# Performance work log

Measured on AMD Instinct MI355X. Metric: run time of the kernel, lower is better.

## Reference

```python
import jax, jax.numpy as jnp
import numpy as np

NUM_NEURONS = 8192
INPUT_SIZE = 512
OUTPUT_SIZE = 512
TAU = 10.0
G = 1.5


def setup_inputs() -> dict:
    key = jax.random.key(0)
    k1, k2, k3, k4, k5 = jax.random.split(key, 5)
    inputs = jax.random.normal(k1, (INPUT_SIZE,), dtype=jnp.float32)
    potentials = jax.random.normal(k2, (1, NUM_NEURONS), dtype=jnp.float32)
    # parameters, matching the torch init scales
    W_in = jax.random.normal(k3, (INPUT_SIZE, NUM_NEURONS), dtype=jnp.float32) * 0.1
    synapses = jax.random.normal(k4, (NUM_NEURONS, NUM_NEURONS), dtype=jnp.float32) / np.sqrt(NUM_NEURONS).astype(np.float32)
    W_out = jax.random.normal(k5, (NUM_NEURONS, OUTPUT_SIZE), dtype=jnp.float32) / np.float32(NUM_NEURONS)
    return {"inputs": inputs, "potentials": potentials, "W_in": W_in,
            "synapses": synapses, "W_out": W_out}


def reference(inputs, potentials, W_in, synapses, W_out):
    # input_map: bias-free linear, then unsqueeze to [1, N]
    drive = (inputs @ W_in)[None, :]                      # [1, N]
    # Neurons: continuous-time leaky integrator (FORCE-style)
    rates = jnp.tanh(potentials)                          # [1, N]
    pot_new = potentials + (-potentials + G * (rates @ synapses) + drive) / TAU
    gen_net = jnp.tanh(pot_new)                           # [1, N]
    # read_out: bias-free linear
    output = gen_net @ W_out                              # [1, output_size]
    return (output, pot_new)
```

## Files before the change

### kernel.cpp

```cpp
#include <hip/hip_runtime.h>
#include <math.h>

#define N_NEU   8192
#define IN_SZ   512
#define OUT_SZ  512
#define N4      (N_NEU / 4)
#define OUT4    (OUT_SZ / 4)
#define KPB     128
#define WPB     8
#define SYN_TILES (N_NEU / KPB)
#define K2_ROWS 64
#define K2_BLKS (N_NEU / K2_ROWS)
constexpr float TAU_INV = 0.1f;
constexpr float G_GAIN  = 1.5f;

__global__ __launch_bounds__(256)
void accum_kernel(const float* __restrict__ pot,
                  const float* __restrict__ inputs,
                  const float* __restrict__ synapses,
                  const float* __restrict__ W_in,
                  float4* __restrict__ P4,
                  float* __restrict__ out) {
    __shared__ float xs[KPB + WPB];
    const int bx = blockIdx.x, by = blockIdx.y;
    const int tid = threadIdx.x;
    const int k0 = by * KPB;
    const int w0 = by * WPB;
    if (tid < KPB)                xs[tid] = G_GAIN * tanhf(pot[k0 + tid]);
    else if (tid < KPB + WPB)     xs[tid] = inputs[w0 + (tid - KPB)];
    if (bx == 0 && by == 0 && tid < 128)
        ((float4*)out)[tid] = make_float4(0.f, 0.f, 0.f, 0.f);
    __syncthreads();

    const int col4 = bx * 256 + tid;
    const float4* Sp = (const float4*)synapses + (size_t)k0 * N4 + col4;
    const float4* Wp = (const float4*)W_in     + (size_t)w0 * N4 + col4;

    float4 acc = make_float4(0.f, 0.f, 0.f, 0.f);
#pragma unroll 8
    for (int i = 0; i < KPB; ++i) {
        float  s = xs[i];
        float4 m = Sp[(size_t)i * N4];
        acc.x = fmaf(s, m.x, acc.x);
        acc.y = fmaf(s, m.y, acc.y);
        acc.z = fmaf(s, m.z, acc.z);
        acc.w = fmaf(s, m.w, acc.w);
    }
#pragma unroll
    for (int i = 0; i < WPB; ++i) {
        float  s = xs[KPB + i];
        float4 m = Wp[(size_t)i * N4];
        acc.x = fmaf(s, m.x, acc.x);
        acc.y = fmaf(s, m.y, acc.y);
        acc.z = fmaf(s, m.z, acc.z);
        acc.w = fmaf(s, m.w, acc.w);
    }
    P4[(size_t)by * N4 + col4] = acc;
}

__global__ __launch_bounds__(256)
void finish_kernel(const float* __restrict__ pot,
                   const float* __restrict__ P,
                   const float* __restrict__ W_out,
                   float* __restrict__ out) {
    __shared__ float  red[256];
    __shared__ float  xs[K2_ROWS];
    __shared__ float4 hi[128];
    const int b = blockIdx.x;
    const int t = threadIdx.x;
    const int k0 = b * K2_ROWS;
    const int r = t & 63;
    const int q = t >> 6;

    float s = 0.f;
#pragma unroll
    for (int p = 0; p < 16; ++p)
        s += P[(size_t)(q * 16 + p) * N_NEU + k0 + r];
    red[t] = s;
    __syncthreads();

    if (t < K2_ROWS) {
        float drive = red[t] + red[64 + t] + red[128 + t] + red[192 + t];
        float pv = pot[k0 + t];
        float pn = pv + (drive - pv) * TAU_INV;
        out[OUT_SZ + k0 + t] = pn;
        xs[t] = tanhf(pn);
    }
    __syncthreads();

    const int c4 = t & 127;
    const int h  = t >> 7;
    const float4* Wp = (const float4*)W_out + (size_t)(k0 + h * 32) * OUT4 + c4;
    float4 acc = make_float4(0.f, 0.f, 0.f, 0.f);
#pragma unroll 8
    for (int i = 0; i < 32; ++i) {
        float  sx = xs[h * 32 + i];
        float4 m  = Wp[(size_t)i * OUT4];
        acc.x = fmaf(sx, m.x, acc.x);
        acc.y = fmaf(sx, m.y, acc.y);
        acc.z = fmaf(sx, m.z, acc.z);
        acc.w = fmaf(sx, m.w, acc.w);
    }
    if (h == 1) hi[c4] = acc;
    __syncthreads();
    if (h == 0) {
        float4 o = hi[c4];
        acc.x += o.x; acc.y += o.y; acc.z += o.z; acc.w += o.w;
        float* op = out + (size_t)c4 * 4;
        atomicAdd(op + 0, acc.x);
        atomicAdd(op + 1, acc.y);
        atomicAdd(op + 2, acc.z);
        atomicAdd(op + 3, acc.w);
    }
}

extern "C" void kernel_launch(void* const* d_in, const int* in_sizes, int n_in,
                              void* d_out, int out_size, void* d_ws, size_t ws_size,
                              hipStream_t stream) {
    const float* inputs   = (const float*)d_in[0];
    const float* pot      = (const float*)d_in[1];
    const float* W_in     = (const float*)d_in[2];
    const float* synapses = (const float*)d_in[3];
    const float* W_out    = (const float*)d_in[4];

    float* out = (float*)d_out;
    float* P   = (float*)d_ws;

    accum_kernel<<<dim3(8, SYN_TILES), dim3(256), 0, stream>>>(
        pot, inputs, synapses, W_in, (float4*)P, out);

    finish_kernel<<<dim3(K2_BLKS), dim3(256), 0, stream>>>(
        pot, P, W_out, out);
}
```

Measured before the change: 392.0 us.

## Restructure synapse GEMV so each block covers full row span over fewer rows

```diff
diff --git a/kernel.cpp b/kernel.cpp
--- a/kernel.cpp
+++ b/kernel.cpp
@@ -6,9 +6,10 @@
 #define OUT_SZ  512
 #define N4      (N_NEU / 4)
 #define OUT4    (OUT_SZ / 4)
-#define KPB     128
-#define WPB     8
-#define SYN_TILES (N_NEU / KPB)
+#define KPB     32
+#define WPB     2
+#define NBLK1   (N_NEU / KPB)
+#define NQ      (N4 / 256)
 #define K2_ROWS 64
 #define K2_BLKS (N_NEU / K2_ROWS)
 constexpr float TAU_INV = 0.1f;
@@ -22,40 +23,51 @@
                   float4* __restrict__ P4,
                   float* __restrict__ out) {
     __shared__ float xs[KPB + WPB];
-    const int bx = blockIdx.x, by = blockIdx.y;
+    const int by = blockIdx.x;
     const int tid = threadIdx.x;
     const int k0 = by * KPB;
     const int w0 = by * WPB;
     if (tid < KPB)                xs[tid] = G_GAIN * tanhf(pot[k0 + tid]);
     else if (tid < KPB + WPB)     xs[tid] = inputs[w0 + (tid - KPB)];
-    if (bx == 0 && by == 0 && tid < 128)
+    if (by == 0 && tid < 128)
         ((float4*)out)[tid] = make_float4(0.f, 0.f, 0.f, 0.f);
     __syncthreads();
 
-    const int col4 = bx * 256 + tid;
-    const float4* Sp = (const float4*)synapses + (size_t)k0 * N4 + col4;
-    const float4* Wp = (const float4*)W_in     + (size_t)w0 * N4 + col4;
+    float4 acc[NQ];
+#pragma unroll
+    for (int j = 0; j < NQ; ++j) acc[j] = make_float4(0.f, 0.f, 0.f, 0.f);
 
-    float4 acc = make_float4(0.f, 0.f, 0.f, 0.f);
-#pragma unroll 8
+    const float4* Sp = (const float4*)synapses + (size_t)k0 * N4 + tid;
+#pragma unroll 2
     for (int i = 0; i < KPB; ++i) {
-        float  s = xs[i];
-        float4 m = Sp[(size_t)i * N4];
-        acc.x = fmaf(s, m.x, acc.x);
-        acc.y = fmaf(s, m.y, acc.y);
-        acc.z = fmaf(s, m.z, acc.z);
-        acc.w = fmaf(s, m.w, acc.w);
+        const float s = xs[i];
+        const float4* row = Sp + (size_t)i * N4;
+#pragma unroll
+        for (int j = 0; j < NQ; ++j) {
+            float4 m = row[j * 256];
+            acc[j].x = fmaf(s, m.x, acc[j].x);
+            acc[j].y = fmaf(s, m.y, acc[j].y);
+            acc[j].z = fmaf(s, m.z, acc[j].z);
+            acc[j].w = fmaf(s, m.w, acc[j].w);
+        }
     }
+    const float4* Wp = (const float4*)W_in + (size_t)w0 * N4 + tid;
 #pragma unroll
     for (int i = 0; i < WPB; ++i) {
-        float  s = xs[KPB + i];
-        float4 m = Wp[(size_t)i * N4];
-        acc.x = fmaf(s, m.x, acc.x);
-        acc.y = fmaf(s, m.y, acc.y);
-        acc.z = fmaf(s, m.z, acc.z);
-        acc.w = fmaf(s, m.w, acc.w);
+        const float s = xs[KPB + i];
+        const float4* row = Wp + (size_t)i * N4;
+#pragma unroll
+        for (int j = 0; j < NQ; ++j) {
+            float4 m = row[j * 256];
+            acc[j].x = fmaf(s, m.x, acc[j].x);
+            acc[j].y = fmaf(s, m.y, acc[j].y);
+            acc[j].z = fmaf(s, m.z, acc[j].z);
+            acc[j].w = fmaf(s, m.w, acc[j].w);
+        }
     }
-    P4[(size_t)by * N4 + col4] = acc;
+    float4* Pp = P4 + (size_t)by * N4 + tid;
+#pragma unroll
+    for (int j = 0; j < NQ; ++j) Pp[j * 256] = acc[j];
 }
 
 __global__ __launch_bounds__(256)
@@ -73,9 +85,9 @@
     const int q = t >> 6;
 
     float s = 0.f;
-#pragma unroll
-    for (int p = 0; p < 16; ++p)
-        s += P[(size_t)(q * 16 + p) * N_NEU + k0 + r];
+#pragma unroll 8
+    for (int p = 0; p < 64; ++p)
+        s += P[(size_t)(q * 64 + p) * N_NEU + k0 + r];
     red[t] = s;
     __syncthreads();
 
@@ -126,7 +138,7 @@
     float* out = (float*)d_out;
     float* P   = (float*)d_ws;
 
-    accum_kernel<<<dim3(8, SYN_TILES), dim3(256), 0, stream>>>(
+    accum_kernel<<<dim3(NBLK1), dim3(256), 0, stream>>>(
         pot, inputs, synapses, W_in, (float4*)P, out);
 
     finish_kernel<<<dim3(K2_BLKS), dim3(256), 0, stream>>>(
```

After: 401.3 us. 2.4% more time.
